# Optimization experiments

Hardware: AMD Instinct MI355X
Metric: run time of the kernel (lower is better)

The kernel has to match this reference:

```python
import jax, jax.numpy as jnp
import numpy as np

NQ, BS, HW, D, H, DFF = 300, 16, 2048, 256, 8, 2048
HD2 = (2 * D) // H   # cross-attn head dim (query/key), 64
VHD = D // H         # value head dim, 32
EPS = 1e-5


def _lin_params(key, din, dout):
    kw, kb = jax.random.split(key)
    w = jax.random.normal(kw, (din, dout), jnp.float32) * 0.02
    b = jax.random.normal(kb, (dout,), jnp.float32) * 0.02
    return w, b


def setup_inputs() -> dict:
    key = jax.random.key(0)
    ks = jax.random.split(key, 24)
    inp = {
        'tgt': jax.random.normal(ks[0], (NQ, BS, D), jnp.float32),
        'memory': jax.random.normal(ks[1], (HW, BS, D), jnp.float32),
        'pos': jax.random.normal(ks[2], (HW, BS, D), jnp.float32),
        'cls_query_pos': jax.random.normal(ks[3], (NQ, BS, D), jnp.float32),
        'cls_query_sine_embed': jax.random.normal(ks[4], (NQ, BS, D), jnp.float32),
    }
    names = [('w_qc', 'b_qc', D, D), ('w_qp', 'b_qp', D, D), ('w_kc', 'b_kc', D, D),
             ('w_kp', 'b_kp', D, D), ('w_v', 'b_v', D, D), ('w_qs', 'b_qs', D, D),
             ('wq', 'bq', 2 * D, 2 * D), ('wk', 'bk', 2 * D, 2 * D),
             ('wv', 'bv', D, D), ('wo', 'bo', D, D),
             ('w1', 'b1', D, DFF), ('w2', 'b2', DFF, D)]
    for i, (wn, bn, din, dout) in enumerate(names):
        w, b = _lin_params(ks[5 + i], din, dout)
        inp[wn], inp[bn] = w, b
    inp['g2'] = jnp.ones((D,), jnp.float32)
    inp['be2'] = jnp.zeros((D,), jnp.float32)
    inp['g3'] = jnp.ones((D,), jnp.float32)
    inp['be3'] = jnp.zeros((D,), jnp.float32)
    return inp


def _ln(x, g, b):
    m = x.mean(-1, keepdims=True)
    v = ((x - m) ** 2).mean(-1, keepdims=True)
    return (x - m) * jax.lax.rsqrt(v + EPS) * g + b


def reference(tgt, memory, pos, cls_query_pos, cls_query_sine_embed,
              w_qc, b_qc, w_qp, b_qp, w_kc, b_kc, w_kp, b_kp, w_v, b_v,
              w_qs, b_qs, wq, bq, wk, bk, wv, bv, wo, bo,
              w1, b1, w2, b2, g2, be2, g3, be3):
    nq, bs, d = tgt.shape
    hw = memory.shape[0]
    # conditional cross-attention projections (is_first=True path)
    q_content = tgt @ w_qc + b_qc
    k_content = memory @ w_kc + b_kc
    v_in = memory @ w_v + b_v
    k_pos = pos @ w_kp + b_kp
    q_pos = cls_query_pos @ w_qp + b_qp
    q = (q_content + q_pos).reshape(nq, bs, H, d // H)
    sine = (cls_query_sine_embed @ w_qs + b_qs).reshape(nq, bs, H, d // H)
    q = jnp.concatenate([q, sine], axis=3).reshape(nq, bs, 2 * d)
    k = (k_content + k_pos).reshape(hw, bs, H, d // H)
    kp = k_pos.reshape(hw, bs, H, d // H)
    k = jnp.concatenate([k, kp], axis=3).reshape(hw, bs, 2 * d)
    # MultiheadAttention(embed_dim=2d, nhead, vdim=d): internal q/k/v/out projs
    scale = 1.0 / jnp.sqrt(jnp.float32(HD2))
    qh = ((q @ wq + bq) * scale).reshape(nq, bs, H, HD2)
    kh = (k @ wk + bk).reshape(hw, bs, H, HD2)
    vh = (v_in @ wv + bv).reshape(hw, bs, H, VHD)
    logits = jnp.einsum('qbhd,kbhd->bhqk', qh, kh)
    attn = jax.nn.softmax(logits, axis=-1)              # [bs, H, nq, hw]
    ctx = jnp.einsum('bhqk,kbhd->qbhd', attn, vh).reshape(nq, bs, d)
    tgt2 = ctx @ wo + bo
    attn_avg = attn.mean(axis=1)                        # averaged over heads
    # residual + norm + FFN + norm (dropout disabled / eval)
    x = _ln(tgt + tgt2, g2, be2)
    ffn = jax.nn.relu(x @ w1 + b1) @ w2 + b2
    x = _ln(x + ffn, g3, be3)
    return (x, attn_avg)
```

## Files before the change

### kernel.cpp

```cpp
#include <hip/hip_runtime.h>

typedef unsigned short u16;
typedef __attribute__((ext_vector_type(8))) short short8;
typedef __attribute__((ext_vector_type(4))) float f32x4;

#define MFMA16(a, b, c) __builtin_amdgcn_mfma_f32_16x16x32_bf16(a, b, c, 0, 0, 0)

__device__ __forceinline__ float bf2f(u16 u) {
    return __uint_as_float(((unsigned)u) << 16);
}
__device__ __forceinline__ u16 f2bf(float f) {
    unsigned u = __float_as_uint(f);
    u += 0x7fff + ((u >> 16) & 1);
    return (u16)(u >> 16);
}

__global__ __launch_bounds__(256) void cvt2(const float* __restrict__ a,
                                            const float* __restrict__ b,
                                            u16* __restrict__ A, u16* __restrict__ B) {
    size_t i = ((size_t)blockIdx.x * 256 + threadIdx.x) * 4;
    float4 va = *(const float4*)(a + i);
    float4 vb = *(const float4*)(b + i);
    u16 ta[4] = {f2bf(va.x), f2bf(va.y), f2bf(va.z), f2bf(va.w)};
    u16 tb[4] = {f2bf(vb.x), f2bf(vb.y), f2bf(vb.z), f2bf(vb.w)};
    *(uint2*)(A + i) = *(uint2*)ta;
    *(uint2*)(B + i) = *(uint2*)tb;
}

__global__ __launch_bounds__(256) void fold_q(const float* __restrict__ w_qc,
                                              const float* __restrict__ w_qp,
                                              const float* __restrict__ w_qs,
                                              const float* __restrict__ wq,
                                              u16* __restrict__ WQ3T) {
    int o = blockIdx.x * 256 + threadIdx.x;
    int k0 = blockIdx.y * 4;
    int seg = k0 >> 8, kb = k0 & 255;
    const float* wsrc = (seg == 0) ? w_qc : ((seg == 1) ? w_qp : w_qs);
    int sOff = (seg == 2) ? 32 : 0;
    const float* wcol = wq + o;
    float acc[4] = {0.f, 0.f, 0.f, 0.f};
#pragma unroll 8
    for (int c = 0; c < 256; c++) {
        int mc = (c >> 5) * 64 + (c & 31) + sOff;
        float w0 = wcol[(size_t)mc * 512];
#pragma unroll
        for (int j = 0; j < 4; j++)
            acc[j] += wsrc[(size_t)(kb + j) * 256 + c] * w0;
    }
    u16 outv[4];
#pragma unroll
    for (int j = 0; j < 4; j++) outv[j] = f2bf(acc[j] * 0.125f);
    *(uint2*)(WQ3T + (size_t)o * 768 + k0) = *(uint2*)outv;
}

__global__ __launch_bounds__(256) void fold_k(const float* __restrict__ w_kc,
                                              const float* __restrict__ w_kp,
                                              const float* __restrict__ wk,
                                              u16* __restrict__ WK2T) {
    int o = blockIdx.x * 256 + threadIdx.x;
    int k0 = blockIdx.y * 4;
    bool second = k0 >= 256;
    int kb = second ? k0 - 256 : k0;
    const float* wcol = wk + o;
    float acc[4] = {0.f, 0.f, 0.f, 0.f};
    if (second) {
#pragma unroll 8
        for (int c = 0; c < 256; c++) {
            int mc = (c >> 5) * 64 + (c & 31);
            float w0 = wcol[(size_t)mc * 512] + wcol[(size_t)(mc + 32) * 512];
#pragma unroll
            for (int j = 0; j < 4; j++)
                acc[j] += w_kp[(size_t)(kb + j) * 256 + c] * w0;
        }
    } else {
#pragma unroll 8
        for (int c = 0; c < 256; c++) {
            int mc = (c >> 5) * 64 + (c & 31);
            float w0 = wcol[(size_t)mc * 512];
#pragma unroll
            for (int j = 0; j < 4; j++)
                acc[j] += w_kc[(size_t)(kb + j) * 256 + c] * w0;
        }
    }
    u16 outv[4];
#pragma unroll
    for (int j = 0; j < 4; j++) outv[j] = f2bf(acc[j]);
    *(uint2*)(WK2T + (size_t)o * 512 + k0) = *(uint2*)outv;
}

__global__ __launch_bounds__(256) void fold_v(const float* __restrict__ w_v,
                                              const float* __restrict__ wv_w,
                                              u16* __restrict__ WV2T) {
    int o = threadIdx.x;
    int k0 = blockIdx.y * 4;
    float acc[4] = {0.f, 0.f, 0.f, 0.f};
#pragma unroll 8
    for (int c = 0; c < 256; c++) {
        float w0 = wv_w[(size_t)c * 256 + o];
#pragma unroll
        for (int j = 0; j < 4; j++)
            acc[j] += w_v[(size_t)(k0 + j) * 256 + c] * w0;
    }
    u16 outv[4];
#pragma unroll
    for (int j = 0; j < 4; j++) outv[j] = f2bf(acc[j]);
    *(uint2*)(WV2T + (size_t)o * 256 + k0) = *(uint2*)outv;
}

__global__ __launch_bounds__(256) void fold_bias(
    const float* b_qc, const float* b_qp, const float* b_qs, const float* wq, const float* bq,
    const float* b_kc, const float* b_kp, const float* wk, const float* bk,
    const float* b_v, const float* wv_w, const float* bv,
    float* BQF, float* BKF, float* BVF) {
    __shared__ float red[4][64];
    int tid = threadIdx.x, lane = tid & 63, wave = tid >> 6;
    int blk = blockIdx.x;
    float acc = 0.f;
    if (blk < 8) {
        int o = blk * 64 + lane;
#pragma unroll 4
        for (int c = wave * 64; c < wave * 64 + 64; c++) {
            int mc = (c >> 5) * 64 + (c & 31);
            acc += (b_qc[c] + b_qp[c]) * wq[(size_t)mc * 512 + o];
            acc += b_qs[c] * wq[(size_t)(mc + 32) * 512 + o];
        }
        red[wave][lane] = acc;
        __syncthreads();
        if (wave == 0)
            BQF[o] = (bq[o] + red[0][lane] + red[1][lane] + red[2][lane] + red[3][lane]) * 0.125f;
    } else if (blk < 16) {
        int o = (blk - 8) * 64 + lane;
#pragma unroll 4
        for (int c = wave * 64; c < wave * 64 + 64; c++) {
            int mc = (c >> 5) * 64 + (c & 31);
            acc += (b_kc[c] + b_kp[c]) * wk[(size_t)mc * 512 + o];
            acc += b_kp[c] * wk[(size_t)(mc + 32) * 512 + o];
        }
        red[wave][lane] = acc;
        __syncthreads();
        if (wave == 0)
            BKF[o] = bk[o] + red[0][lane] + red[1][lane] + red[2][lane] + red[3][lane];
    } else {
        int o = (blk - 16) * 64 + lane;
#pragma unroll 4
        for (int c = wave * 64; c < wave * 64 + 64; c++)
            acc += b_v[c] * wv_w[(size_t)c * 256 + o];
        red[wave][lane] = acc;
        __syncthreads();
        if (wave == 0)
            BVF[o] = bv[o] + red[0][lane] + red[1][lane] + red[2][lane] + red[3][lane];
    }
}

__global__ __launch_bounds__(256) void transpose_f2b(const float* __restrict__ src,
                                                     u16* __restrict__ dst, int R, int C) {
    __shared__ float tile[32][33];
    int c0 = blockIdx.x * 32, r0 = blockIdx.y * 32;
    int t = threadIdx.x;
    int j = t & 31, i0 = (t >> 5) * 4;
#pragma unroll
    for (int ii = 0; ii < 4; ii++)
        tile[i0 + ii][j] = src[(size_t)(r0 + i0 + ii) * C + c0 + j];
    __syncthreads();
    int i2 = t & 31, j0 = (t >> 5) * 4;
#pragma unroll
    for (int jj = 0; jj < 4; jj++)
        dst[(size_t)(c0 + j0 + jj) * R + r0 + i2] = f2bf(tile[i2][j0 + jj]);
}

#define APAD 40
__global__ __launch_bounds__(256) void gemm_bt(
    const void* __restrict__ A0v, const void* __restrict__ A1v, const void* __restrict__ A2v,
    int astride, int a_f32, const u16* __restrict__ BT, const float* __restrict__ bias,
    u16* __restrict__ C, int M, int N, int K, int mode) {
    __shared__ u16 As[128 * APAD];
    __shared__ u16 Bs[128 * APAD];
    int tid = threadIdx.x;
    int wave = tid >> 6, lane = tid & 63;
    int l15 = lane & 15, quad = lane >> 4;
    int wm = (wave >> 1) * 64, wn = (wave & 1) * 64;
    int gm0 = blockIdx.y * 128, gn0 = blockIdx.x * 128;
    f32x4 acc[4][4] = {};
    for (int k0 = 0; k0 < K; k0 += 32) {
        const void* ap;
        int kin;
        if (astride == 256) {
            int p = k0 >> 8;
            ap = (p == 0) ? A0v : ((p == 1) ? A1v : A2v);
            kin = k0 & 255;
        } else {
            ap = A0v;
            kin = k0;
        }
#pragma unroll
        for (int i = 0; i < 2; i++) {
            int idx = tid * 2 + i;
            int row = idx >> 2, seg = (idx & 3) * 8;
            int grow = gm0 + row;
            u16 tmp[8];
            if (a_f32) {
                float vv[8] = {0.f, 0.f, 0.f, 0.f, 0.f, 0.f, 0.f, 0.f};
                if (grow < M) {
                    const float* apf = (const float*)ap;
                    float4 u0 = *(const float4*)(apf + (size_t)grow * astride + kin + seg);
                    float4 u1 = *(const float4*)(apf + (size_t)grow * astride + kin + seg + 4);
                    vv[0] = u0.x; vv[1] = u0.y; vv[2] = u0.z; vv[3] = u0.w;
                    vv[4] = u1.x; vv[5] = u1.y; vv[6] = u1.z; vv[7] = u1.w;
                }
#pragma unroll
                for (int e = 0; e < 8; e++) tmp[e] = f2bf(vv[e]);
            } else {
                uint4 v;
                v.x = v.y = v.z = v.w = 0;
                if (grow < M) v = *(const uint4*)((const u16*)ap + (size_t)grow * astride + kin + seg);
                *(uint4*)tmp = v;
            }
            *(uint4*)(&As[row * APAD + seg]) = *(uint4*)tmp;
            int nrow = gn0 + row;
            uint4 w = *(const uint4*)(BT + (size_t)nrow * K + k0 + seg);
            *(uint4*)(&Bs[row * APAD + seg]) = w;
        }
        __syncthreads();
        short8 afr[4], bfr[4];
#pragma unroll
        for (int i = 0; i < 4; i++)
            afr[i] = *(const short8*)(&As[(wm + i * 16 + l15) * APAD + quad * 8]);
#pragma unroll
        for (int j = 0; j < 4; j++)
            bfr[j] = *(const short8*)(&Bs[(wn + j * 16 + l15) * APAD + quad * 8]);
#pragma unroll
        for (int i = 0; i < 4; i++)
#pragma unroll
            for (int j = 0; j < 4; j++) acc[i][j] = MFMA16(afr[i], bfr[j], acc[i][j]);
        __syncthreads();
    }
#pragma unroll
    for (int i = 0; i < 4; i++) {
        int row = gm0 + wm + i * 16 + quad * 4;
#pragma unroll
        for (int j = 0; j < 4; j++) {
            int col = gn0 + wn + j * 16 + l15;
            float bvv = bias[col];
#pragma unroll
            for (int r = 0; r < 4; r++) {
                int grow = row + r;
                if (grow < M) {
                    float v = acc[i][j][r] + bvv;
                    if (mode == 1) v = fmaxf(v, 0.f);
                    C[(size_t)grow * N + col] = f2bf(v);
                }
            }
        }
    }
}

__global__ __launch_bounds__(256) void attn_a(const u16* __restrict__ qh,
                                              const u16* __restrict__ kh,
                                              const u16* __restrict__ vhr,
                                              u16* __restrict__ ctxbuf,
                                              float* __restrict__ z8inv) {
    int qt = blockIdx.x, h = blockIdx.y, b = blockIdx.z;
    __shared__ u16 Qt[64 * 72];
    __shared__ u16 Kc[128 * 72];
    __shared__ u16 Pt[64 * 136];
    __shared__ u16 VTc[32 * 136];
    int tid = threadIdx.x, wave = tid >> 6, lane = tid & 63;
    int l15 = lane & 15, quad = lane >> 4;
    int q0 = qt * 64;
#pragma unroll
    for (int i = 0; i < 2; i++) {
        int idx = tid * 2 + i;
        int row = idx >> 3, seg = (idx & 7) * 8;
        uint4 v;
        v.x = v.y = v.z = v.w = 0;
        int q = q0 + row;
        if (q < 300) v = *(const uint4*)(qh + ((size_t)q * 16 + b) * 512 + h * 64 + seg);
        *(uint4*)(&Qt[row * 72 + seg]) = v;
    }
    const f32x4 zf = {0.f, 0.f, 0.f, 0.f};
    f32x4 cacc[2] = {};
    float zl = 0.f;
    for (int kc0 = 0; kc0 < 2048; kc0 += 128) {
#pragma unroll
        for (int i = 0; i < 4; i++) {
            int idx = tid * 4 + i;
            int row = idx >> 3, seg = (idx & 7) * 8;
            *(uint4*)(&Kc[row * 72 + seg]) =
                *(const uint4*)(kh + ((size_t)(kc0 + row) * 16 + b) * 512 + h * 64 + seg);
        }
#pragma unroll
        for (int i = 0; i < 2; i++) {
            int idx = tid * 2 + i;
            int kk = idx >> 2, dseg = (idx & 3) * 8;
            u16 tmp[8];
            *(uint4*)tmp = *(const uint4*)(vhr + ((size_t)(kc0 + kk) * 16 + b) * 256 + h * 32 + dseg);
#pragma unroll
            for (int e = 0; e < 8; e++) VTc[(dseg + e) * 136 + kk] = tmp[e];
        }
        __syncthreads();
        f32x4 sacc[8];
#pragma unroll
        for (int t = 0; t < 8; t++) sacc[t] = zf;
#pragma unroll
        for (int d0 = 0; d0 < 64; d0 += 32) {
            short8 bfq = *(const short8*)(&Qt[(wave * 16 + l15) * 72 + d0 + quad * 8]);
#pragma unroll
            for (int t = 0; t < 8; t++) {
                short8 afk = *(const short8*)(&Kc[(t * 16 + l15) * 72 + d0 + quad * 8]);
                sacc[t] = MFMA16(afk, bfq, sacc[t]);
            }
        }
#pragma unroll
        for (int t = 0; t < 8; t++) {
            u16 pk[4];
#pragma unroll
            for (int r = 0; r < 4; r++) {
                float p = __expf(sacc[t][r]);
                zl += p;
                pk[r] = f2bf(p);
            }
            *(uint2*)(&Pt[(wave * 16 + l15) * 136 + t * 16 + quad * 4]) = *(uint2*)pk;
        }
#pragma unroll
        for (int kk0 = 0; kk0 < 128; kk0 += 32) {
            short8 af = *(const short8*)(&Pt[(wave * 16 + l15) * 136 + kk0 + quad * 8]);
#pragma unroll
            for (int t = 0; t < 2; t++) {
                short8 bf = *(const short8*)(&VTc[(t * 16 + l15) * 136 + kk0 + quad * 8]);
                cacc[t] = MFMA16(af, bf, cacc[t]);
            }
        }
        __syncthreads();
    }
    zl += __shfl_xor(zl, 16);
    zl += __shfl_xor(zl, 32);
    {
        int q = q0 + wave * 16 + l15;
        if (quad == 0 && q < 300) z8inv[((size_t)b * 8 + h) * 320 + q] = 0.125f / zl;
    }
#pragma unroll
    for (int r = 0; r < 4; r++) {
        int q = q0 + wave * 16 + quad * 4 + r;
        if (q < 300) {
            float rz = 1.0f / __shfl(zl, quad * 4 + r);
#pragma unroll
            for (int t = 0; t < 2; t++)
                ctxbuf[((size_t)q * 16 + b) * 256 + h * 32 + t * 16 + l15] = f2bf(cacc[t][r] * rz);
        }
    }
}

__global__ __launch_bounds__(256) void attn_b(const u16* __restrict__ qh,
                                              const u16* __restrict__ kh,
                                              const float* __restrict__ z8inv,
                                              float* __restrict__ out1) {
    int kc0 = blockIdx.x * 128, qt = blockIdx.y, b = blockIdx.z;
    __shared__ u16 Qt[64 * 72];
    __shared__ u16 Kc[128 * 72];
    int tid = threadIdx.x, wave = tid >> 6, lane = tid & 63;
    int l15 = lane & 15, quad = lane >> 4;
    int q0 = qt * 64;
    int qme = q0 + wave * 16 + l15;
    const f32x4 zf = {0.f, 0.f, 0.f, 0.f};
    f32x4 avg[8] = {};
    for (int h = 0; h < 8; h++) {
#pragma unroll
        for (int i = 0; i < 2; i++) {
            int idx = tid * 2 + i;
            int row = idx >> 3, seg = (idx & 7) * 8;
            uint4 v;
            v.x = v.y = v.z = v.w = 0;
            int q = q0 + row;
            if (q < 300) v = *(const uint4*)(qh + ((size_t)q * 16 + b) * 512 + h * 64 + seg);
            *(uint4*)(&Qt[row * 72 + seg]) = v;
        }
#pragma unroll
        for (int i = 0; i < 4; i++) {
            int idx = tid * 4 + i;
            int row = idx >> 3, seg = (idx & 7) * 8;
            *(uint4*)(&Kc[row * 72 + seg]) =
                *(const uint4*)(kh + ((size_t)(kc0 + row) * 16 + b) * 512 + h * 64 + seg);
        }
        __syncthreads();
        f32x4 sacc[8];
#pragma unroll
        for (int t = 0; t < 8; t++) sacc[t] = zf;
#pragma unroll
        for (int d0 = 0; d0 < 64; d0 += 32) {
            short8 bfq = *(const short8*)(&Qt[(wave * 16 + l15) * 72 + d0 + quad * 8]);
#pragma unroll
            for (int t = 0; t < 8; t++) {
                short8 afk = *(const short8*)(&Kc[(t * 16 + l15) * 72 + d0 + quad * 8]);
                sacc[t] = MFMA16(afk, bfq, sacc[t]);
            }
        }
        float zi = z8inv[((size_t)b * 8 + h) * 320 + (qme < 319 ? qme : 319)];
#pragma unroll
        for (int t = 0; t < 8; t++)
#pragma unroll
            for (int r = 0; r < 4; r++) avg[t][r] += __expf(sacc[t][r]) * zi;
        __syncthreads();
    }
    if (qme < 300) {
        float* op = out1 + ((size_t)b * 300 + qme) * 2048 + kc0 + quad * 4;
#pragma unroll
        for (int t = 0; t < 8; t++)
            *(float4*)(op + t * 16) = *(float4*)(&avg[t]);
    }
}

__global__ __launch_bounds__(256) void ln_kernel(const void* __restrict__ a, int a_f32,
                                                 const u16* __restrict__ bres,
                                                 const float* __restrict__ g,
                                                 const float* __restrict__ be,
                                                 void* __restrict__ out, int out_f32) {
    int row = blockIdx.x, t = threadIdx.x;
    float av = a_f32 ? ((const float*)a)[(size_t)row * 256 + t]
                     : bf2f(((const u16*)a)[(size_t)row * 256 + t]);
    float v = av + bf2f(bres[(size_t)row * 256 + t]);
    float s = v, sq = v * v;
#pragma unroll
    for (int o = 32; o; o >>= 1) {
        s += __shfl_xor(s, o);
        sq += __shfl_xor(sq, o);
    }
    __shared__ float red[8];
    int wave = t >> 6, lane = t & 63;
    if (lane == 0) {
        red[wave] = s;
        red[4 + wave] = sq;
    }
    __syncthreads();
    s = red[0] + red[1] + red[2] + red[3];
    sq = red[4] + red[5] + red[6] + red[7];
    float mean = s * (1.f / 256.f);
    float var = sq * (1.f / 256.f) - mean * mean;
    float rs = rsqrtf(var + 1e-5f);
    float res = (v - mean) * rs * g[t] + be[t];
    if (out_f32) ((float*)out)[(size_t)row * 256 + t] = res;
    else ((u16*)out)[(size_t)row * 256 + t] = f2bf(res);
}

extern "C" void kernel_launch(void* const* d_in, const int* in_sizes, int n_in,
                              void* d_out, int out_size, void* d_ws, size_t ws_size,
                              hipStream_t stream) {
    (void)in_sizes; (void)n_in; (void)out_size; (void)ws_size;
    const float* tgt = (const float*)d_in[0];
    const float* mem = (const float*)d_in[1];
    const float* pos = (const float*)d_in[2];
    const float* qpos = (const float*)d_in[3];
    const float* qsine = (const float*)d_in[4];
    const float* w_qc = (const float*)d_in[5];
    const float* b_qc = (const float*)d_in[6];
    const float* w_qp = (const float*)d_in[7];
    const float* b_qp = (const float*)d_in[8];
    const float* w_kc = (const float*)d_in[9];
    const float* b_kc = (const float*)d_in[10];
    const float* w_kp = (const float*)d_in[11];
    const float* b_kp = (const float*)d_in[12];
    const float* w_v = (const float*)d_in[13];
    const float* b_v = (const float*)d_in[14];
    const float* w_qs = (const float*)d_in[15];
    const float* b_qs = (const float*)d_in[16];
    const float* wq = (const float*)d_in[17];
    const float* bq = (const float*)d_in[18];
    const float* wk = (const float*)d_in[19];
    const float* bk = (const float*)d_in[20];
    const float* wv_w = (const float*)d_in[21];
    const float* bv = (const float*)d_in[22];
    const float* wo = (const float*)d_in[23];
    const float* bo = (const float*)d_in[24];
    const float* w1 = (const float*)d_in[25];
    const float* b1 = (const float*)d_in[26];
    const float* w2 = (const float*)d_in[27];
    const float* b2 = (const float*)d_in[28];
    const float* g2 = (const float*)d_in[29];
    const float* be2 = (const float*)d_in[30];
    const float* g3 = (const float*)d_in[31];
    const float* be3 = (const float*)d_in[32];

    char* ws = (char*)d_ws;
    u16* WQ3T = (u16*)(ws + 0x000000);
    u16* WK2T = (u16*)(ws + 0x0C0000);
    u16* WV2T = (u16*)(ws + 0x140000);
    u16* WOT  = (u16*)(ws + 0x160000);
    u16* W1T  = (u16*)(ws + 0x180000);
    u16* W2T  = (u16*)(ws + 0x280000);
    float* BQF = (float*)(ws + 0x380000);
    float* BKF = (float*)(ws + 0x381000);
    float* BVF = (float*)(ws + 0x382000);
    float* Z8  = (float*)(ws + 0x390000);
    u16* QH  = (u16*)(ws + 0x400000);
    u16* KH  = (u16*)(ws + 0x900000);
    u16* CTX = (u16*)(ws + 0x2900000);
    u16* TGT2 = (u16*)(ws + 0x900000);
    u16* XBUF = (u16*)(ws + 0xB60000);
    u16* FFNB = (u16*)(ws + 0xDC0000);
    u16* HBUF = (u16*)(ws + 0x1020000);

    float* out0 = (float*)d_out;
    float* out1 = out0 + 1228800;
    u16* MB  = (u16*)out1;
    u16* PB  = MB + 8388608;
    u16* VHR = PB;

    cvt2<<<8192, 256, 0, stream>>>(mem, pos, MB, PB);
    fold_q<<<dim3(2, 192), 256, 0, stream>>>(w_qc, w_qp, w_qs, wq, WQ3T);
    fold_k<<<dim3(2, 128), 256, 0, stream>>>(w_kc, w_kp, wk, WK2T);
    fold_v<<<dim3(1, 64), 256, 0, stream>>>(w_v, wv_w, WV2T);
    fold_bias<<<20, 256, 0, stream>>>(b_qc, b_qp, b_qs, wq, bq, b_kc, b_kp, wk, bk,
                                      b_v, wv_w, bv, BQF, BKF, BVF);
    transpose_f2b<<<dim3(8, 8), 256, 0, stream>>>(wo, WOT, 256, 256);
    transpose_f2b<<<dim3(64, 8), 256, 0, stream>>>(w1, W1T, 256, 2048);
    transpose_f2b<<<dim3(8, 64), 256, 0, stream>>>(w2, W2T, 2048, 256);

    gemm_bt<<<dim3(4, 38), 256, 0, stream>>>(tgt, qpos, qsine, 256, 1, WQ3T, BQF, QH, 4800, 512, 768, 0);
    gemm_bt<<<dim3(4, 256), 256, 0, stream>>>(MB, PB, nullptr, 256, 0, WK2T, BKF, KH, 32768, 512, 512, 0);
    gemm_bt<<<dim3(2, 256), 256, 0, stream>>>(MB, nullptr, nullptr, 256, 0, WV2T, BVF, VHR, 32768, 256, 256, 0);

    attn_a<<<dim3(5, 8, 16), 256, 0, stream>>>(QH, KH, VHR, CTX, Z8);
    attn_b<<<dim3(16, 5, 16), 256, 0, stream>>>(QH, KH, Z8, out1);

    gemm_bt<<<dim3(2, 38), 256, 0, stream>>>(CTX, nullptr, nullptr, 256, 0, WOT, bo, TGT2, 4800, 256, 256, 0);
    ln_kernel<<<4800, 256, 0, stream>>>(tgt, 1, TGT2, g2, be2, XBUF, 0);
    gemm_bt<<<dim3(16, 38), 256, 0, stream>>>(XBUF, nullptr, nullptr, 256, 0, W1T, b1, HBUF, 4800, 2048, 256, 1);
    gemm_bt<<<dim3(2, 38), 256, 0, stream>>>(HBUF, nullptr, nullptr, 2048, 0, W2T, b2, FFNB, 4800, 256, 2048, 0);
    ln_kernel<<<4800, 256, 0, stream>>>(XBUF, 0, FFNB, g3, be3, out0, 1);
}
```

Before: 603.9 us.

## Process 112 queries per attn_a block and reorder grids for K/V locality

attn_a now covers 112 query rows per block in two 64-row passes over each loaded K/V chunk, cutting the grid from 5x8x16 to 128x3. Each K/V tile fetched from global memory is therefore reused by more queries, so K/V traffic and block count drop. It adds an extra barrier per pass, more LDS for the larger Q tile, and fewer blocks (384) for the GPU to spread across its CUs. attn_b's grid is flattened so batch varies fastest across consecutive blocks, which changes which tiles run concurrently and how they share cache.

```diff
diff --git a/kernel.cpp b/kernel.cpp
--- a/kernel.cpp
+++ b/kernel.cpp
@@ -259,27 +259,29 @@
                                               const u16* __restrict__ vhr,
                                               u16* __restrict__ ctxbuf,
                                               float* __restrict__ z8inv) {
-    int qt = blockIdx.x, h = blockIdx.y, b = blockIdx.z;
-    __shared__ u16 Qt[64 * 72];
+    int hb = blockIdx.x, qs = blockIdx.y;
+    int h = hb & 7, b = hb >> 3;
+    int q0 = qs * 112;
+    __shared__ u16 Qt[128 * 72];
     __shared__ u16 Kc[128 * 72];
     __shared__ u16 Pt[64 * 136];
     __shared__ u16 VTc[32 * 136];
     int tid = threadIdx.x, wave = tid >> 6, lane = tid & 63;
     int l15 = lane & 15, quad = lane >> 4;
-    int q0 = qt * 64;
-#pragma unroll
-    for (int i = 0; i < 2; i++) {
-        int idx = tid * 2 + i;
+#pragma unroll
+    for (int i = 0; i < 4; i++) {
+        int idx = tid + 256 * i;
         int row = idx >> 3, seg = (idx & 7) * 8;
         uint4 v;
         v.x = v.y = v.z = v.w = 0;
         int q = q0 + row;
-        if (q < 300) v = *(const uint4*)(qh + ((size_t)q * 16 + b) * 512 + h * 64 + seg);
+        if (row < 112 && q < 300)
+            v = *(const uint4*)(qh + ((size_t)q * 16 + b) * 512 + h * 64 + seg);
         *(uint4*)(&Qt[row * 72 + seg]) = v;
     }
     const f32x4 zf = {0.f, 0.f, 0.f, 0.f};
-    f32x4 cacc[2] = {};
-    float zl = 0.f;
+    f32x4 cacc[2][2] = {};
+    float zl[2] = {0.f, 0.f};
     for (int kc0 = 0; kc0 < 2048; kc0 += 128) {
 #pragma unroll
         for (int i = 0; i < 4; i++) {
@@ -298,54 +300,67 @@
             for (int e = 0; e < 8; e++) VTc[(dseg + e) * 136 + kk] = tmp[e];
         }
         __syncthreads();
-        f32x4 sacc[8];
-#pragma unroll
-        for (int t = 0; t < 8; t++) sacc[t] = zf;
-#pragma unroll
-        for (int d0 = 0; d0 < 64; d0 += 32) {
-            short8 bfq = *(const short8*)(&Qt[(wave * 16 + l15) * 72 + d0 + quad * 8]);
+#pragma unroll
+        for (int pass = 0; pass < 2; pass++) {
+            int R0 = pass * 64;
+            f32x4 sacc[8];
+#pragma unroll
+            for (int t = 0; t < 8; t++) sacc[t] = zf;
+#pragma unroll
+            for (int d0 = 0; d0 < 64; d0 += 32) {
+                short8 bfq = *(const short8*)(&Qt[(R0 + wave * 16 + l15) * 72 + d0 + quad * 8]);
+#pragma unroll
+                for (int t = 0; t < 8; t++) {
+                    short8 afk = *(const short8*)(&Kc[(t * 16 + l15) * 72 + d0 + quad * 8]);
+                    sacc[t] = MFMA16(afk, bfq, sacc[t]);
+                }
+            }
 #pragma unroll
             for (int t = 0; t < 8; t++) {
-                short8 afk = *(const short8*)(&Kc[(t * 16 + l15) * 72 + d0 + quad * 8]);
-                sacc[t] = MFMA16(afk, bfq, sacc[t]);
-            }
-        }
-#pragma unroll
-        for (int t = 0; t < 8; t++) {
-            u16 pk[4];
-#pragma unroll
-            for (int r = 0; r < 4; r++) {
-                float p = __expf(sacc[t][r]);
-                zl += p;
-                pk[r] = f2bf(p);
-            }
-            *(uint2*)(&Pt[(wave * 16 + l15) * 136 + t * 16 + quad * 4]) = *(uint2*)pk;
-        }
-#pragma unroll
-        for (int kk0 = 0; kk0 < 128; kk0 += 32) {
-            short8 af = *(const short8*)(&Pt[(wave * 16 + l15) * 136 + kk0 + quad * 8]);
-#pragma unroll
-            for (int t = 0; t < 2; t++) {
-                short8 bf = *(const short8*)(&VTc[(t * 16 + l15) * 136 + kk0 + quad * 8]);
-                cacc[t] = MFMA16(af, bf, cacc[t]);
-            }
-        }
-        __syncthreads();
-    }
-    zl += __shfl_xor(zl, 16);
-    zl += __shfl_xor(zl, 32);
-    {
-        int q = q0 + wave * 16 + l15;
-        if (quad == 0 && q < 300) z8inv[((size_t)b * 8 + h) * 320 + q] = 0.125f / zl;
-    }
-#pragma unroll
-    for (int r = 0; r < 4; r++) {
-        int q = q0 + wave * 16 + quad * 4 + r;
-        if (q < 300) {
-            float rz = 1.0f / __shfl(zl, quad * 4 + r);
-#pragma unroll
-            for (int t = 0; t < 2; t++)
-                ctxbuf[((size_t)q * 16 + b) * 256 + h * 32 + t * 16 + l15] = f2bf(cacc[t][r] * rz);
+                u16 pk[4];
+#pragma unroll
+                for (int r = 0; r < 4; r++) {
+                    float p = __expf(sacc[t][r]);
+                    zl[pass] += p;
+                    pk[r] = f2bf(p);
+                }
+                *(uint2*)(&Pt[(wave * 16 + l15) * 136 + t * 16 + quad * 4]) = *(uint2*)pk;
+            }
+            __syncthreads();
+#pragma unroll
+            for (int kk0 = 0; kk0 < 128; kk0 += 32) {
+                short8 af = *(const short8*)(&Pt[(wave * 16 + l15) * 136 + kk0 + quad * 8]);
+#pragma unroll
+                for (int t = 0; t < 2; t++) {
+                    short8 bf = *(const short8*)(&VTc[(t * 16 + l15) * 136 + kk0 + quad * 8]);
+                    cacc[pass][t] = MFMA16(af, bf, cacc[pass][t]);
+                }
+            }
+            __syncthreads();
+        }
+    }
+#pragma unroll
+    for (int pass = 0; pass < 2; pass++) {
+        int R0 = pass * 64;
+        float z = zl[pass];
+        z += __shfl_xor(z, 16);
+        z += __shfl_xor(z, 32);
+        {
+            int lr = R0 + wave * 16 + l15;
+            int q = q0 + lr;
+            if (quad == 0 && lr < 112 && q < 300)
+                z8inv[((size_t)b * 8 + h) * 320 + q] = 0.125f / z;
+        }
+#pragma unroll
+        for (int r = 0; r < 4; r++) {
+            int lr = R0 + wave * 16 + quad * 4 + r;
+            int q = q0 + lr;
+            if (lr < 112 && q < 300) {
+                float rz = 1.0f / __shfl(z, quad * 4 + r);
+#pragma unroll
+                for (int t = 0; t < 2; t++)
+                    ctxbuf[((size_t)q * 16 + b) * 256 + h * 32 + t * 16 + l15] = f2bf(cacc[pass][t][r] * rz);
+            }
         }
     }
 }
@@ -354,7 +369,7 @@
                                               const u16* __restrict__ kh,
                                               const float* __restrict__ z8inv,
                                               float* __restrict__ out1) {
-    int kc0 = blockIdx.x * 128, qt = blockIdx.y, b = blockIdx.z;
+    int kc0 = (blockIdx.x >> 4) * 128, b = blockIdx.x & 15, qt = blockIdx.y;
     __shared__ u16 Qt[64 * 72];
     __shared__ u16 Kc[128 * 72];
     int tid = threadIdx.x, wave = tid >> 6, lane = tid & 63;
@@ -518,8 +533,8 @@
     gemm_bt<<<dim3(4, 256), 256, 0, stream>>>(MB, PB, nullptr, 256, 0, WK2T, BKF, KH, 32768, 512, 512, 0);
     gemm_bt<<<dim3(2, 256), 256, 0, stream>>>(MB, nullptr, nullptr, 256, 0, WV2T, BVF, VHR, 32768, 256, 256, 0);
 
-    attn_a<<<dim3(5, 8, 16), 256, 0, stream>>>(QH, KH, VHR, CTX, Z8);
-    attn_b<<<dim3(16, 5, 16), 256, 0, stream>>>(QH, KH, Z8, out1);
+    attn_a<<<dim3(128, 3), 256, 0, stream>>>(QH, KH, VHR, CTX, Z8);
+    attn_b<<<dim3(256, 5), 256, 0, stream>>>(QH, KH, Z8, out1);
 
     gemm_bt<<<dim3(2, 38), 256, 0, stream>>>(CTX, nullptr, nullptr, 256, 0, WOT, bo, TGT2, 4800, 256, 256, 0);
     ln_kernel<<<4800, 256, 0, stream>>>(tgt, 1, TGT2, g2, be2, XBUF, 0);
```

After: 599.2 us. No clear change (-0.8%).

## Split attention over key chunks with combine kernel; add wider-tile GEMM; reorder attn_b grid

Applied to the files above, without the earlier changes.

attn_a now splits the 2048 keys into four 512-key slices per (batch, head), and each block loops over all five query tiles. It writes unnormalised partial context and partial softmax denominators, and a new attn_comb kernel sums them, normalises, and writes ctx and the inverse-z values. A new gemm_bt2 with 128x256 tiles replaces the old GEMM for the Q, K, V and FFN1 projections, aiming for more data reuse per block. attn_b's grid is flattened so that batch varies fastest. The partials are stored in bf16 in reused output scratch, which adds memory traffic and a small precision loss.

```diff
diff --git a/kernel.cpp b/kernel.cpp
--- a/kernel.cpp
+++ b/kernel.cpp
@@ -254,107 +254,219 @@
     }
 }
 
+__global__ __launch_bounds__(256) void gemm_bt2(
+    const void* __restrict__ A0v, const void* __restrict__ A1v, const void* __restrict__ A2v,
+    int astride, int a_f32, const u16* __restrict__ BT, const float* __restrict__ bias,
+    u16* __restrict__ C, int M, int N, int K, int mode) {
+    __shared__ u16 As[128 * APAD];
+    __shared__ u16 Bs[256 * APAD];
+    int tid = threadIdx.x;
+    int wave = tid >> 6, lane = tid & 63;
+    int l15 = lane & 15, quad = lane >> 4;
+    int wm = (wave >> 1) * 64, wn = (wave & 1) * 128;
+    int gm0 = blockIdx.y * 128, gn0 = blockIdx.x * 256;
+    f32x4 acc[4][8] = {};
+    for (int k0 = 0; k0 < K; k0 += 32) {
+        const void* ap;
+        int kin;
+        if (astride == 256) {
+            int p = k0 >> 8;
+            ap = (p == 0) ? A0v : ((p == 1) ? A1v : A2v);
+            kin = k0 & 255;
+        } else {
+            ap = A0v;
+            kin = k0;
+        }
+#pragma unroll
+        for (int i = 0; i < 2; i++) {
+            int idx = tid * 2 + i;
+            int row = idx >> 2, seg = (idx & 3) * 8;
+            int grow = gm0 + row;
+            u16 tmp[8];
+            if (a_f32) {
+                float vv[8] = {0.f, 0.f, 0.f, 0.f, 0.f, 0.f, 0.f, 0.f};
+                if (grow < M) {
+                    const float* apf = (const float*)ap;
+                    float4 u0 = *(const float4*)(apf + (size_t)grow * astride + kin + seg);
+                    float4 u1 = *(const float4*)(apf + (size_t)grow * astride + kin + seg + 4);
+                    vv[0] = u0.x; vv[1] = u0.y; vv[2] = u0.z; vv[3] = u0.w;
+                    vv[4] = u1.x; vv[5] = u1.y; vv[6] = u1.z; vv[7] = u1.w;
+                }
+#pragma unroll
+                for (int e = 0; e < 8; e++) tmp[e] = f2bf(vv[e]);
+            } else {
+                uint4 v;
+                v.x = v.y = v.z = v.w = 0;
+                if (grow < M) v = *(const uint4*)((const u16*)ap + (size_t)grow * astride + kin + seg);
+                *(uint4*)tmp = v;
+            }
+            *(uint4*)(&As[row * APAD + seg]) = *(uint4*)tmp;
+        }
+#pragma unroll
+        for (int i = 0; i < 4; i++) {
+            int idx = tid * 4 + i;
+            int row = idx >> 2, seg = (idx & 3) * 8;
+            uint4 w = *(const uint4*)(BT + (size_t)(gn0 + row) * K + k0 + seg);
+            *(uint4*)(&Bs[row * APAD + seg]) = w;
+        }
+        __syncthreads();
+        short8 afr[4], bfr[8];
+#pragma unroll
+        for (int i = 0; i < 4; i++)
+            afr[i] = *(const short8*)(&As[(wm + i * 16 + l15) * APAD + quad * 8]);
+#pragma unroll
+        for (int j = 0; j < 8; j++)
+            bfr[j] = *(const short8*)(&Bs[(wn + j * 16 + l15) * APAD + quad * 8]);
+#pragma unroll
+        for (int i = 0; i < 4; i++)
+#pragma unroll
+            for (int j = 0; j < 8; j++) acc[i][j] = MFMA16(afr[i], bfr[j], acc[i][j]);
+        __syncthreads();
+    }
+#pragma unroll
+    for (int i = 0; i < 4; i++) {
+        int row = gm0 + wm + i * 16 + quad * 4;
+#pragma unroll
+        for (int j = 0; j < 8; j++) {
+            int col = gn0 + wn + j * 16 + l15;
+            float bvv = bias[col];
+#pragma unroll
+            for (int r = 0; r < 4; r++) {
+                int grow = row + r;
+                if (grow < M) {
+                    float v = acc[i][j][r] + bvv;
+                    if (mode == 1) v = fmaxf(v, 0.f);
+                    C[(size_t)grow * N + col] = f2bf(v);
+                }
+            }
+        }
+    }
+}
+
 __global__ __launch_bounds__(256) void attn_a(const u16* __restrict__ qh,
                                               const u16* __restrict__ kh,
                                               const u16* __restrict__ vhr,
-                                              u16* __restrict__ ctxbuf,
-                                              float* __restrict__ z8inv) {
-    int qt = blockIdx.x, h = blockIdx.y, b = blockIdx.z;
+                                              u16* __restrict__ CPB,
+                                              float* __restrict__ ZPF) {
+    int hb = blockIdx.x, s = blockIdx.y;
+    int h = hb & 7, b = hb >> 3;
     __shared__ u16 Qt[64 * 72];
     __shared__ u16 Kc[128 * 72];
     __shared__ u16 Pt[64 * 136];
     __shared__ u16 VTc[32 * 136];
     int tid = threadIdx.x, wave = tid >> 6, lane = tid & 63;
     int l15 = lane & 15, quad = lane >> 4;
-    int q0 = qt * 64;
-#pragma unroll
-    for (int i = 0; i < 2; i++) {
-        int idx = tid * 2 + i;
-        int row = idx >> 3, seg = (idx & 7) * 8;
-        uint4 v;
-        v.x = v.y = v.z = v.w = 0;
-        int q = q0 + row;
-        if (q < 300) v = *(const uint4*)(qh + ((size_t)q * 16 + b) * 512 + h * 64 + seg);
-        *(uint4*)(&Qt[row * 72 + seg]) = v;
-    }
+    size_t pbase = ((size_t)(s * 16 + b) * 8 + h);
     const f32x4 zf = {0.f, 0.f, 0.f, 0.f};
-    f32x4 cacc[2] = {};
-    float zl = 0.f;
-    for (int kc0 = 0; kc0 < 2048; kc0 += 128) {
-#pragma unroll
-        for (int i = 0; i < 4; i++) {
-            int idx = tid * 4 + i;
-            int row = idx >> 3, seg = (idx & 7) * 8;
-            *(uint4*)(&Kc[row * 72 + seg]) =
-                *(const uint4*)(kh + ((size_t)(kc0 + row) * 16 + b) * 512 + h * 64 + seg);
-        }
+    for (int qt = 0; qt < 5; qt++) {
+        int q0 = qt * 64;
 #pragma unroll
         for (int i = 0; i < 2; i++) {
             int idx = tid * 2 + i;
-            int kk = idx >> 2, dseg = (idx & 3) * 8;
-            u16 tmp[8];
-            *(uint4*)tmp = *(const uint4*)(vhr + ((size_t)(kc0 + kk) * 16 + b) * 256 + h * 32 + dseg);
-#pragma unroll
-            for (int e = 0; e < 8; e++) VTc[(dseg + e) * 136 + kk] = tmp[e];
-        }
-        __syncthreads();
-        f32x4 sacc[8];
-#pragma unroll
-        for (int t = 0; t < 8; t++) sacc[t] = zf;
-#pragma unroll
-        for (int d0 = 0; d0 < 64; d0 += 32) {
-            short8 bfq = *(const short8*)(&Qt[(wave * 16 + l15) * 72 + d0 + quad * 8]);
+            int row = idx >> 3, seg = (idx & 7) * 8;
+            uint4 v;
+            v.x = v.y = v.z = v.w = 0;
+            int q = q0 + row;
+            if (q < 300) v = *(const uint4*)(qh + ((size_t)q * 16 + b) * 512 + h * 64 + seg);
+            *(uint4*)(&Qt[row * 72 + seg]) = v;
+        }
+        f32x4 cacc[2] = {};
+        float zl = 0.f;
+        for (int c = 0; c < 4; c++) {
+            int kc0 = s * 512 + c * 128;
+#pragma unroll
+            for (int i = 0; i < 4; i++) {
+                int idx = tid * 4 + i;
+                int row = idx >> 3, seg = (idx & 7) * 8;
+                *(uint4*)(&Kc[row * 72 + seg]) =
+                    *(const uint4*)(kh + ((size_t)(kc0 + row) * 16 + b) * 512 + h * 64 + seg);
+            }
+#pragma unroll
+            for (int i = 0; i < 2; i++) {
+                int idx = tid * 2 + i;
+                int kk = idx >> 2, dseg = (idx & 3) * 8;
+                u16 tmp[8];
+                *(uint4*)tmp = *(const uint4*)(vhr + ((size_t)(kc0 + kk) * 16 + b) * 256 + h * 32 + dseg);
+#pragma unroll
+                for (int e = 0; e < 8; e++) VTc[(dseg + e) * 136 + kk] = tmp[e];
+            }
+            __syncthreads();
+            f32x4 sacc[8];
+#pragma unroll
+            for (int t = 0; t < 8; t++) sacc[t] = zf;
+#pragma unroll
+            for (int d0 = 0; d0 < 64; d0 += 32) {
+                short8 bfq = *(const short8*)(&Qt[(wave * 16 + l15) * 72 + d0 + quad * 8]);
+#pragma unroll
+                for (int t = 0; t < 8; t++) {
+                    short8 afk = *(const short8*)(&Kc[(t * 16 + l15) * 72 + d0 + quad * 8]);
+                    sacc[t] = MFMA16(afk, bfq, sacc[t]);
+                }
+            }
 #pragma unroll
             for (int t = 0; t < 8; t++) {
-                short8 afk = *(const short8*)(&Kc[(t * 16 + l15) * 72 + d0 + quad * 8]);
-                sacc[t] = MFMA16(afk, bfq, sacc[t]);
-            }
-        }
-#pragma unroll
-        for (int t = 0; t < 8; t++) {
-            u16 pk[4];
-#pragma unroll
-            for (int r = 0; r < 4; r++) {
-                float p = __expf(sacc[t][r]);
-                zl += p;
-                pk[r] = f2bf(p);
-            }
-            *(uint2*)(&Pt[(wave * 16 + l15) * 136 + t * 16 + quad * 4]) = *(uint2*)pk;
-        }
-#pragma unroll
-        for (int kk0 = 0; kk0 < 128; kk0 += 32) {
-            short8 af = *(const short8*)(&Pt[(wave * 16 + l15) * 136 + kk0 + quad * 8]);
-#pragma unroll
-            for (int t = 0; t < 2; t++) {
-                short8 bf = *(const short8*)(&VTc[(t * 16 + l15) * 136 + kk0 + quad * 8]);
-                cacc[t] = MFMA16(af, bf, cacc[t]);
-            }
-        }
-        __syncthreads();
-    }
-    zl += __shfl_xor(zl, 16);
-    zl += __shfl_xor(zl, 32);
-    {
-        int q = q0 + wave * 16 + l15;
-        if (quad == 0 && q < 300) z8inv[((size_t)b * 8 + h) * 320 + q] = 0.125f / zl;
-    }
-#pragma unroll
-    for (int r = 0; r < 4; r++) {
-        int q = q0 + wave * 16 + quad * 4 + r;
-        if (q < 300) {
-            float rz = 1.0f / __shfl(zl, quad * 4 + r);
-#pragma unroll
-            for (int t = 0; t < 2; t++)
-                ctxbuf[((size_t)q * 16 + b) * 256 + h * 32 + t * 16 + l15] = f2bf(cacc[t][r] * rz);
-        }
-    }
+                u16 pk[4];
+#pragma unroll
+                for (int r = 0; r < 4; r++) {
+                    float p = __expf(sacc[t][r]);
+                    zl += p;
+                    pk[r] = f2bf(p);
+                }
+                *(uint2*)(&Pt[(wave * 16 + l15) * 136 + t * 16 + quad * 4]) = *(uint2*)pk;
+            }
+#pragma unroll
+            for (int kk0 = 0; kk0 < 128; kk0 += 32) {
+                short8 af = *(const short8*)(&Pt[(wave * 16 + l15) * 136 + kk0 + quad * 8]);
+#pragma unroll
+                for (int t = 0; t < 2; t++) {
+                    short8 bf = *(const short8*)(&VTc[(t * 16 + l15) * 136 + kk0 + quad * 8]);
+                    cacc[t] = MFMA16(af, bf, cacc[t]);
+                }
+            }
+            __syncthreads();
+        }
+        float z = zl;
+        z += __shfl_xor(z, 16);
+        z += __shfl_xor(z, 32);
+        {
+            int q = q0 + wave * 16 + l15;
+            if (quad == 0 && q < 300) ZPF[pbase * 300 + q] = z;
+        }
+#pragma unroll
+        for (int r = 0; r < 4; r++) {
+            int q = q0 + wave * 16 + quad * 4 + r;
+            if (q < 300) {
+#pragma unroll
+                for (int t = 0; t < 2; t++)
+                    CPB[(pbase * 300 + q) * 32 + t * 16 + l15] = f2bf(cacc[t][r]);
+            }
+        }
+    }
+}
+
+__global__ __launch_bounds__(256) void attn_comb(const u16* __restrict__ CPB,
+                                                 const float* __restrict__ ZPF,
+                                                 u16* __restrict__ ctxbuf,
+                                                 float* __restrict__ z8inv) {
+    int q = blockIdx.x, b = blockIdx.y;
+    int tid = threadIdx.x;
+    int h = tid >> 5, d = tid & 31;
+    float z = 0.f, c = 0.f;
+#pragma unroll
+    for (int s = 0; s < 4; s++) {
+        size_t pbase = ((size_t)(s * 16 + b) * 8 + h);
+        z += ZPF[pbase * 300 + q];
+        c += bf2f(CPB[(pbase * 300 + q) * 32 + d]);
+    }
+    ctxbuf[((size_t)q * 16 + b) * 256 + h * 32 + d] = f2bf(c / z);
+    if (d == 0) z8inv[((size_t)b * 8 + h) * 320 + q] = 0.125f / z;
 }
 
 __global__ __launch_bounds__(256) void attn_b(const u16* __restrict__ qh,
                                               const u16* __restrict__ kh,
                                               const float* __restrict__ z8inv,
                                               float* __restrict__ out1) {
-    int kc0 = blockIdx.x * 128, qt = blockIdx.y, b = blockIdx.z;
+    int kc0 = (blockIdx.x >> 4) * 128, b = blockIdx.x & 15, qt = blockIdx.y;
     __shared__ u16 Qt[64 * 72];
     __shared__ u16 Kc[128 * 72];
     int tid = threadIdx.x, wave = tid >> 6, lane = tid & 63;
@@ -503,6 +615,8 @@
     u16* MB  = (u16*)out1;
     u16* PB  = MB + 8388608;
     u16* VHR = PB;
+    u16* CPB = MB;
+    float* ZPF = (float*)((char*)out1 + 0xA00000);
 
     cvt2<<<8192, 256, 0, stream>>>(mem, pos, MB, PB);
     fold_q<<<dim3(2, 192), 256, 0, stream>>>(w_qc, w_qp, w_qs, wq, WQ3T);
@@ -514,16 +628,17 @@
     transpose_f2b<<<dim3(64, 8), 256, 0, stream>>>(w1, W1T, 256, 2048);
     transpose_f2b<<<dim3(8, 64), 256, 0, stream>>>(w2, W2T, 2048, 256);
 
-    gemm_bt<<<dim3(4, 38), 256, 0, stream>>>(tgt, qpos, qsine, 256, 1, WQ3T, BQF, QH, 4800, 512, 768, 0);
-    gemm_bt<<<dim3(4, 256), 256, 0, stream>>>(MB, PB, nullptr, 256, 0, WK2T, BKF, KH, 32768, 512, 512, 0);
-    gemm_bt<<<dim3(2, 256), 256, 0, stream>>>(MB, nullptr, nullptr, 256, 0, WV2T, BVF, VHR, 32768, 256, 256, 0);
-
-    attn_a<<<dim3(5, 8, 16), 256, 0, stream>>>(QH, KH, VHR, CTX, Z8);
-    attn_b<<<dim3(16, 5, 16), 256, 0, stream>>>(QH, KH, Z8, out1);
+    gemm_bt2<<<dim3(2, 38), 256, 0, stream>>>(tgt, qpos, qsine, 256, 1, WQ3T, BQF, QH, 4800, 512, 768, 0);
+    gemm_bt2<<<dim3(2, 256), 256, 0, stream>>>(MB, PB, nullptr, 256, 0, WK2T, BKF, KH, 32768, 512, 512, 0);
+    gemm_bt2<<<dim3(1, 256), 256, 0, stream>>>(MB, nullptr, nullptr, 256, 0, WV2T, BVF, VHR, 32768, 256, 256, 0);
+
+    attn_a<<<dim3(128, 4), 256, 0, stream>>>(QH, KH, VHR, CPB, ZPF);
+    attn_comb<<<dim3(300, 16), 256, 0, stream>>>(CPB, ZPF, CTX, Z8);
+    attn_b<<<dim3(256, 5), 256, 0, stream>>>(QH, KH, Z8, out1);
 
     gemm_bt<<<dim3(2, 38), 256, 0, stream>>>(CTX, nullptr, nullptr, 256, 0, WOT, bo, TGT2, 4800, 256, 256, 0);
     ln_kernel<<<4800, 256, 0, stream>>>(tgt, 1, TGT2, g2, be2, XBUF, 0);
-    gemm_bt<<<dim3(16, 38), 256, 0, stream>>>(XBUF, nullptr, nullptr, 256, 0, W1T, b1, HBUF, 4800, 2048, 256, 1);
+    gemm_bt2<<<dim3(8, 38), 256, 0, stream>>>(XBUF, nullptr, nullptr, 256, 0, W1T, b1, HBUF, 4800, 2048, 256, 1);
     gemm_bt<<<dim3(2, 38), 256, 0, stream>>>(HBUF, nullptr, nullptr, 2048, 0, W2T, b2, FFNB, 4800, 256, 2048, 0);
     ln_kernel<<<4800, 256, 0, stream>>>(XBUF, 0, FFNB, g3, be3, out0, 1);
 }
```

Result: slower. 666.0 us (+10.3%).
